# Performance work log

Measured on AMD Instinct MI355X. Metric: run time of the kernel, lower is better.

The kernel has to match this reference:

```python
import jax, jax.numpy as jnp
import numpy as np

N_NODES = 50000
N_EDGES = 800000
D_IN = 128
D_OUT = 128
N_GRAPHS = 512
N_CONVS = 5
EPS = 1e-5


def setup_inputs() -> dict:
    key = jax.random.key(0)
    ks = jax.random.split(key, 8)
    x = jax.random.normal(ks[0], (N_NODES, D_IN), dtype=jnp.float32)
    edge_index = jax.random.randint(ks[1], (2, N_EDGES), 0, N_NODES, dtype=jnp.int32)
    batch = jnp.sort(jax.random.randint(ks[2], (N_NODES,), 0, N_GRAPHS, dtype=jnp.int32))
    s = 1.0 / np.sqrt(D_IN)
    W_rel = jax.random.normal(ks[3], (N_CONVS, D_OUT, D_IN), dtype=jnp.float32) * s
    b_rel = jax.random.normal(ks[4], (N_CONVS, D_OUT), dtype=jnp.float32) * s
    W_root = jax.random.normal(ks[5], (N_CONVS, D_OUT, D_IN), dtype=jnp.float32) * s
    gamma = jnp.ones((D_OUT,), dtype=jnp.float32)
    beta = jnp.zeros((D_OUT,), dtype=jnp.float32)
    Wc = jax.random.normal(ks[6], (96, D_OUT), dtype=jnp.float32) * (1.0 / np.sqrt(D_OUT))
    bc = jax.random.normal(ks[7], (96,), dtype=jnp.float32) * (1.0 / np.sqrt(D_OUT))
    return {"x": x, "edge_index": edge_index, "batch": batch, "i": 0,
            "W_rel": W_rel, "b_rel": b_rel, "W_root": W_root,
            "gamma": gamma, "beta": beta, "Wc": Wc, "bc": bc}


def reference(x, edge_index, batch, i, W_rel, b_rel, W_root, gamma, beta, Wc, bc):
    # --- 5 GraphConv branches, summed. GraphConv: lin_rel(sum_{j->i} x_j) + lin_root(x).
    # Sum over the 5 convs commutes with the linears, so fold the weights first.
    src, dst = edge_index[0], edge_index[1]
    agg = jax.ops.segment_sum(x[src], dst, num_segments=N_NODES)  # [N, D_in]
    Wr = jnp.sum(W_rel, axis=0)   # [D_out, D_in]
    Wt = jnp.sum(W_root, axis=0)  # [D_out, D_in]
    br = jnp.sum(b_rel, axis=0)   # [D_out]
    h = agg @ Wr.T + x @ Wt.T + br  # [N, D_out]
    # --- NodeLevelBatchNorm (training: batch stats over all nodes, biased var)
    mean = jnp.mean(h, axis=0)
    var = jnp.mean((h - mean) ** 2, axis=0)
    h = gamma * (h - mean) * jax.lax.rsqrt(var + EPS) + beta
    # --- global max pool over graphs, relu, classifier (i=0 -> no-dropout branch)
    pooled = jax.ops.segment_max(h, batch, num_segments=N_GRAPHS)  # [G, D_out]
    pooled = jax.nn.relu(pooled)
    return pooled @ Wc.T + bc  # [G, 96]
```

## Files before the change

### kernel.cpp

```cpp
#include <hip/hip_runtime.h>

#define EPS 1e-5f

constexpr int NN = 50000, NE = 800000, DD = 128, NG = 512, NC = 5, NO = 96;
constexpr int MAXB = 8192;
constexpr int NBUCK = 196;

typedef __attribute__((ext_vector_type(8))) short bf16x8;
typedef __attribute__((ext_vector_type(4))) float f32x4;

constexpr size_t HB   = 0;
constexpr size_t XB   = (size_t)NN * DD / 2;
constexpr size_t WB   = XB + (size_t)NN * DD / 2;
constexpr size_t BRO  = WB + DD * 256 / 2;
constexpr size_t CSUM = BRO + DD;
constexpr size_t CSQ  = CSUM + 4 * DD;
constexpr size_t POOL = CSQ + 4 * DD;
constexpr size_t ZLEN = 8 * DD + (size_t)NG * DD;
constexpr size_t GCNT = POOL + (size_t)NG * DD;
constexpr size_t ROFF = GCNT + 256;
constexpr size_t BSTOR= ROFF + NN + 1;
constexpr size_t CSR16= BSTOR + (size_t)NBUCK*MAXB;

constexpr int XCAST_B = NN * DD / 4 / 256;
constexpr int FOLD_B  = DD * DD / 256;
constexpr int BUCK_B  = (NE + 4095) / 4096;

static __device__ __forceinline__ unsigned short f2b(float f) {
    unsigned int u = __float_as_uint(f);
    return (unsigned short)((u + 0x7FFFu + ((u >> 16) & 1u)) >> 16);
}
static __device__ __forceinline__ float b2f(unsigned short h) {
    return __uint_as_float(((unsigned int)h) << 16);
}
static __device__ __forceinline__ unsigned fkey(float f) {
    unsigned u = __float_as_uint(f);
    return (u >> 31) ? ~u : (u | 0x80000000u);
}
static __device__ __forceinline__ float unfkey(unsigned k) {
    unsigned u = (k & 0x80000000u) ? (k ^ 0x80000000u) : ~k;
    return __uint_as_float(u);
}

__global__ __launch_bounds__(256) void k_prep(const float* __restrict__ x,
                                              const float* __restrict__ Wrel,
                                              const float* __restrict__ brel,
                                              const float* __restrict__ Wroot,
                                              const int* __restrict__ ei,
                                              float* __restrict__ ws, int* __restrict__ wi) {
    __shared__ int lcnt[256];
    __shared__ int lbase[256];
    int b = blockIdx.x, t = threadIdx.x;
    if (b < XCAST_B) {
        int i = b * 256 + t;
        float4 v = ((const float4*)x)[i];
        ushort4 o = {f2b(v.x), f2b(v.y), f2b(v.z), f2b(v.w)};
        ((ushort4*)(ws + XB))[i] = o;
    } else if (b < XCAST_B + FOLD_B) {
        int idx = (b - XCAST_B) * 256 + t;
        int k = idx >> 7, o = idx & 127;
        float wr = 0.f, wt = 0.f;
        for (int c = 0; c < NC; ++c) {
            wr += Wrel [c*DD*DD + o*DD + k];
            wt += Wroot[c*DD*DD + o*DD + k];
        }
        unsigned short* wb = (unsigned short*)(ws + WB);
        wb[o*256 + k]       = f2b(wr);
        wb[o*256 + 128 + k] = f2b(wt);
        if (k == 0) {
            float bias = 0.f;
            for (int c = 0; c < NC; ++c) bias += brel[c*DD + o];
            ws[BRO + o] = bias;
        }
    } else {
        int bb = b - XCAST_B - FOLD_B;
        lcnt[t] = 0;
        __syncthreads();
        int val[16], krk[16];
        #pragma unroll
        for (int j = 0; j < 16; ++j) {
            int e = bb * 4096 + j * 256 + t;
            krk[j] = -1;
            if (e < NE) {
                int d = ei[NE + e], s = ei[e];
                int key = d >> 8;
                int r = atomicAdd(&lcnt[key], 1);
                val[j] = s | ((d & 255) << 16);
                krk[j] = (key << 16) | r;
            }
        }
        __syncthreads();
        if (t < NBUCK && lcnt[t] > 0)
            lbase[t] = atomicAdd(&wi[GCNT + t], lcnt[t]);
        __syncthreads();
        #pragma unroll
        for (int j = 0; j < 16; ++j) {
            if (krk[j] >= 0) {
                int key = krk[j] >> 16, r = krk[j] & 0xFFFF;
                int p = lbase[key] + r;
                if (p < MAXB) wi[BSTOR + (size_t)key * MAXB + p] = val[j];
            }
        }
    }
}

__global__ __launch_bounds__(256) void k_sort(int* __restrict__ wi) {
    __shared__ int eds[MAXB];
    __shared__ unsigned short srt[MAXB];
    __shared__ int cnt[256], cnt2[256], lscan[256], gall[256];
    int t = threadIdx.x, b = blockIdx.x;
    for (size_t i = (size_t)b * 256 + t; i < ZLEN; i += (size_t)NBUCK * 256)
        wi[CSUM + i] = 0;
    int g = wi[GCNT + t];
    gall[t] = g; lscan[t] = g; cnt[t] = 0;
    __syncthreads();
    for (int off = 1; off < 256; off <<= 1) {
        int u = (t >= off) ? gall[t - off] : 0;
        __syncthreads();
        gall[t] += u;
        __syncthreads();
    }
    int base = gall[b] - lscan[b];
    int C = lscan[b]; if (C > MAXB) C = MAXB;
    __syncthreads();
    for (int i = t; i < C; i += 256) {
        int v = wi[BSTOR + (size_t)b * MAXB + i];
        eds[i] = v;
        atomicAdd(&cnt[v >> 16], 1);
    }
    __syncthreads();
    int cv = cnt[t];
    for (int off = 1; off < 256; off <<= 1) {
        int u = (t >= off) ? cnt[t - off] : 0;
        __syncthreads();
        cnt[t] += u;
        __syncthreads();
    }
    lscan[t] = cnt[t] - cv;
    cnt2[t] = 0;
    __syncthreads();
    int n = b * 256 + t;
    if (n < NN) wi[ROFF + n] = base + lscan[t];
    if (b == 0 && t == 0) wi[ROFF + NN] = NE;
    for (int i = t; i < C; i += 256) {
        int v = eds[i], k = v >> 16;
        int p = lscan[k] + atomicAdd(&cnt2[k], 1);
        srt[p] = (unsigned short)(v & 0xFFFF);
    }
    __syncthreads();
    unsigned short* csr = (unsigned short*)(wi + CSR16);
    for (int i = t; i < C; i += 256)
        csr[base + i] = srt[i];
}

__global__ __launch_bounds__(256) void k_gather(const int* __restrict__ wi,
                                                float* __restrict__ ws) {
    const unsigned short* xb = (const unsigned short*)(ws + XB);
    const unsigned short* csr = (const unsigned short*)(wi + CSR16);
    unsigned short* hb = (unsigned short*)(ws + HB);
    int tid = threadIdx.x;
    int n   = blockIdx.x * 16 + (tid >> 4);
    int sub = tid & 15;
    int c8  = sub * 8;
    if (n >= NN) return;
    int e0 = wi[ROFF + n], e1 = wi[ROFF + n + 1];
    int cnt = e1 - e0;
    float acc0[8] = {}, acc1[8] = {};
    int base = 0;
    for (; base + 16 <= cnt; base += 16) {
        int myE = (int)csr[e0 + base + sub];
        #pragma unroll
        for (int h = 0; h < 2; ++h) {
            bf16x8 v[8];
            #pragma unroll
            for (int j = 0; j < 8; ++j) {
                int s = __shfl(myE, h * 8 + j, 16);
                v[j] = *(const bf16x8*)&xb[(size_t)s * DD + c8];
            }
            #pragma unroll
            for (int j = 0; j < 8; ++j)
                #pragma unroll
                for (int c = 0; c < 8; ++c)
                    ((j & 1) ? acc1 : acc0)[c] += b2f((unsigned short)v[j][c]);
        }
    }
    int rem = cnt - base;
    if (rem > 0) {
        int myE = (sub < rem) ? (int)csr[e0 + base + sub] : 0;
        int j = 0;
        for (; j + 8 <= rem; j += 8) {
            bf16x8 v[8];
            #pragma unroll
            for (int q = 0; q < 8; ++q) {
                int s = __shfl(myE, j + q, 16);
                v[q] = *(const bf16x8*)&xb[(size_t)s * DD + c8];
            }
            #pragma unroll
            for (int q = 0; q < 8; ++q)
                #pragma unroll
                for (int c = 0; c < 8; ++c)
                    ((q & 1) ? acc1 : acc0)[c] += b2f((unsigned short)v[q][c]);
        }
        if (j + 4 <= rem) {
            bf16x8 v[4];
            #pragma unroll
            for (int q = 0; q < 4; ++q) {
                int s = __shfl(myE, j + q, 16);
                v[q] = *(const bf16x8*)&xb[(size_t)s * DD + c8];
            }
            #pragma unroll
            for (int q = 0; q < 4; ++q)
                #pragma unroll
                for (int c = 0; c < 8; ++c)
                    ((q & 1) ? acc1 : acc0)[c] += b2f((unsigned short)v[q][c]);
            j += 4;
        }
        for (; j < rem; ++j) {
            int s = __shfl(myE, j, 16);
            bf16x8 v = *(const bf16x8*)&xb[(size_t)s * DD + c8];
            #pragma unroll
            for (int c = 0; c < 8; ++c) acc0[c] += b2f((unsigned short)v[c]);
        }
    }
    bf16x8 o;
    #pragma unroll
    for (int c = 0; c < 8; ++c) o[c] = (short)f2b(acc0[c] + acc1[c]);
    *(bf16x8*)&hb[(size_t)n * DD + c8] = o;
}

__global__ __launch_bounds__(256, 2) void k_gemm(const int* __restrict__ batch,
                                                 float* __restrict__ ws) {
    __shared__ __align__(16) unsigned short Bs[DD * 256];
    __shared__ float sSum[128], sSq[128];
    __shared__ int batchS[64];
    __shared__ unsigned maxS[8][128];
    const unsigned short* hb = (const unsigned short*)(ws + HB);
    const unsigned short* xb = (const unsigned short*)(ws + XB);
    unsigned* poolU = (unsigned*)(ws + POOL);
    int tid  = threadIdx.x;
    {
        const float4* wbg = (const float4*)(ws + WB);
        #pragma unroll
        for (int i = 0; i < 16; ++i) {
            int idx = i * 256 + tid;
            float4 v = wbg[idx];
            int byte = idx << 4;
            int col  = byte >> 9;
            int swb  = byte ^ ((col & 7) << 4);
            *(float4*)((char*)Bs + swb) = v;
        }
    }
    if (tid < 128) { sSum[tid] = 0.f; sSq[tid] = 0.f; }
    for (int i = tid; i < 8 * 128; i += 256) ((unsigned*)maxS)[i] = 0u;
    if (tid < 64) {
        int r = blockIdx.x * 64 + tid; if (r > NN - 1) r = NN - 1;
        batchS[tid] = batch[r];
    }
    __syncthreads();
    int gBase = batchS[0];
    int wave = tid >> 6, lane = tid & 63;
    int quad = lane >> 4, l16 = lane & 15;
    int cw = wave * 32;
    auto ldb = [&](int col, int kt) -> bf16x8 {
        int byte = (col << 9) + (kt << 6) + (quad << 4);
        byte ^= ((col & 7) << 4);
        return *(const bf16x8*)((const char*)Bs + byte);
    };
    float bias[2] = { ws[BRO + cw + l16], ws[BRO + cw + 16 + l16] };
    float csum[2] = {}, csq[2] = {};
    #pragma unroll
    for (int rt = 0; rt < 4; ++rt) {
        int lbase = rt * 16;
        int row0 = blockIdx.x * 64 + lbase;
        int arow = row0 + l16; if (arow > NN - 1) arow = NN - 1;
        const unsigned short* aggRow = hb + (size_t)arow * DD;
        const unsigned short* xRow   = xb + (size_t)arow * DD;
        bf16x8 af[8];
        #pragma unroll
        for (int kt = 0; kt < 8; ++kt)
            af[kt] = *(const bf16x8*)((kt < 4 ? aggRow + kt*32 : xRow + kt*32 - 128) + quad*8);
        f32x4 acc[2] = {};
        #pragma unroll
        for (int kt = 0; kt < 8; ++kt) {
            bf16x8 b0 = ldb(cw + l16, kt);
            bf16x8 b1 = ldb(cw + 16 + l16, kt);
            acc[0] = __builtin_amdgcn_mfma_f32_16x16x32_bf16(af[kt], b0, acc[0], 0, 0, 0);
            acc[1] = __builtin_amdgcn_mfma_f32_16x16x32_bf16(af[kt], b1, acc[1], 0, 0, 0);
        }
        #pragma unroll
        for (int nt = 0; nt < 2; ++nt) {
            int col = cw + nt*16 + l16;
            #pragma unroll
            for (int r = 0; r < 4; ++r) {
                int lrow = lbase + quad*4 + r;
                int row  = row0 + quad*4 + r;
                float m = (row < NN) ? 1.f : 0.f;
                float v = acc[nt][r] + bias[nt];
                csum[nt] += v * m;
                csq[nt]  += v * v * m;
                int g   = batchS[lrow];
                int rel = g - gBase;
                unsigned key = (row < NN) ? fkey(v) : 0u;
                if (rel < 8) atomicMax(&maxS[rel][col], key);
                else         atomicMax(&poolU[(size_t)g * DD + col], key);
            }
        }
    }
    __syncthreads();
    int span = batchS[63] - gBase + 1; if (span > 8) span = 8;
    for (int i = tid; i < span * 128; i += 256) {
        unsigned k = maxS[i >> 7][i & 127];
        if (k) atomicMax(&poolU[(size_t)(gBase + (i >> 7)) * DD + (i & 127)], k);
    }
    #pragma unroll
    for (int nt = 0; nt < 2; ++nt) {
        int col = cw + nt*16 + l16;
        float cs = csum[nt], cq = csq[nt];
        cs += __shfl_xor(cs, 16); cs += __shfl_xor(cs, 32);
        cq += __shfl_xor(cq, 16); cq += __shfl_xor(cq, 32);
        if (quad == 0) { atomicAdd(&sSum[col], cs); atomicAdd(&sSq[col], cq); }
    }
    __syncthreads();
    if (tid < 128) {
        int slot = (blockIdx.x & 3) * DD;
        atomicAdd(&ws[CSUM + slot + tid], sSum[tid]);
        atomicAdd(&ws[CSQ  + slot + tid], sSq[tid]);
    }
}

__global__ __launch_bounds__(128) void k_out(const float* __restrict__ gamma,
                                             const float* __restrict__ beta,
                                             const float* __restrict__ Wc,
                                             const float* __restrict__ bc,
                                             const float* __restrict__ ws,
                                             float* __restrict__ out) {
    __shared__ float pS[128];
    int g = blockIdx.x, t = threadIdx.x;
    float s = ws[CSUM + t] + ws[CSUM + DD + t] + ws[CSUM + 2*DD + t] + ws[CSUM + 3*DD + t];
    float q = ws[CSQ  + t] + ws[CSQ  + DD + t] + ws[CSQ  + 2*DD + t] + ws[CSQ  + 3*DD + t];
    float mean = s * (1.0f / NN);
    float var  = q * (1.0f / NN) - mean * mean;
    float sc   = gamma[t] * rsqrtf(var + EPS);
    float sh   = beta[t] - sc * mean;
    unsigned k = ((const unsigned*)(ws + POOL))[(size_t)g * DD + t];
    float p = 0.f;
    if (k) p = fmaxf(unfkey(k) * sc + sh, 0.f);
    pS[t] = p;
    __syncthreads();
    if (t < NO) {
        float acc = bc[t];
        #pragma unroll 8
        for (int kk = 0; kk < DD; ++kk) acc += pS[kk] * Wc[t*DD + kk];
        out[g*NO + t] = acc;
    }
}

extern "C" void kernel_launch(void* const* d_in, const int* in_sizes, int n_in,
                              void* d_out, int out_size, void* d_ws, size_t ws_size,
                              hipStream_t stream) {
    const float* x     = (const float*)d_in[0];
    const int*   ei    = (const int*)  d_in[1];
    const int*   batch = (const int*)  d_in[2];
    const float* Wrel  = (const float*)d_in[4];
    const float* brel  = (const float*)d_in[5];
    const float* Wroot = (const float*)d_in[6];
    const float* gamma = (const float*)d_in[7];
    const float* beta  = (const float*)d_in[8];
    const float* Wc    = (const float*)d_in[9];
    const float* bc    = (const float*)d_in[10];
    float* ws  = (float*)d_ws;
    int*   wi  = (int*)d_ws;
    float* out = (float*)d_out;

    hipMemsetAsync(wi + GCNT, 0, 256 * sizeof(int), stream);

    k_prep  <<<XCAST_B + FOLD_B + BUCK_B, 256, 0, stream>>>(x, Wrel, brel, Wroot, ei, ws, wi);
    k_sort  <<<NBUCK, 256, 0, stream>>>(wi);
    k_gather<<<(NN + 15)/16, 256, 0, stream>>>(wi, ws);
    k_gemm  <<<(NN + 63)/64, 256, 0, stream>>>(batch, ws);
    k_out   <<<NG, 128, 0, stream>>>(gamma, beta, Wc, bc, ws, out);
}
```

Before: 181.1 us.

## Replace global bucket atomics with per-block count matrix and fuse output into GEMM tail

Edge bucketing no longer uses global atomic counters plus a memset. Each prep block writes its per-bucket counts into a 2D matrix and stores its edges in fixed-capacity slots. The sort kernel sums and scans these counts and finds each edge's source slot with a binary search. The final classifier kernel is folded into the GEMM kernel: the last 32 blocks to finish wait on a done counter and then compute the normalized pooled outputs. This removes one launch and the memset, at the cost of spin-waiting and silently dropping edges if a block's bucket count exceeds the 64-slot capacity.

```diff
diff --git a/kernel.cpp b/kernel.cpp
--- a/kernel.cpp
+++ b/kernel.cpp
@@ -5,6 +5,10 @@
 constexpr int NN = 50000, NE = 800000, DD = 128, NG = 512, NC = 5, NO = 96;
 constexpr int MAXB = 8192;
 constexpr int NBUCK = 196;
+constexpr int NPB   = 196;
+constexpr int CAP   = 64;
+constexpr int GEMM_V= (NN + 63) / 64;
+constexpr int FIN   = 32;
 
 typedef __attribute__((ext_vector_type(8))) short bf16x8;
 typedef __attribute__((ext_vector_type(4))) float f32x4;
@@ -16,11 +20,12 @@
 constexpr size_t CSUM = BRO + DD;
 constexpr size_t CSQ  = CSUM + 4 * DD;
 constexpr size_t POOL = CSQ + 4 * DD;
-constexpr size_t ZLEN = 8 * DD + (size_t)NG * DD;
-constexpr size_t GCNT = POOL + (size_t)NG * DD;
-constexpr size_t ROFF = GCNT + 256;
+constexpr size_t DONE = POOL + (size_t)NG * DD;
+constexpr size_t ZLEN = 8 * DD + (size_t)NG * DD + 8;
+constexpr size_t ROFF = DONE + 8;
 constexpr size_t BSTOR= ROFF + NN + 1;
-constexpr size_t CSR16= BSTOR + (size_t)NBUCK*MAXB;
+constexpr size_t CNT2D= BSTOR + (size_t)NBUCK * NPB * CAP;
+constexpr size_t CSR16= CNT2D + (size_t)NPB * 256;
 
 constexpr int XCAST_B = NN * DD / 4 / 256;
 constexpr int FOLD_B  = DD * DD / 256;
@@ -49,7 +54,6 @@
                                               const int* __restrict__ ei,
                                               float* __restrict__ ws, int* __restrict__ wi) {
     __shared__ int lcnt[256];
-    __shared__ int lbase[256];
     int b = blockIdx.x, t = threadIdx.x;
     if (b < XCAST_B) {
         int i = b * 256 + t;
@@ -90,15 +94,16 @@
             }
         }
         __syncthreads();
-        if (t < NBUCK && lcnt[t] > 0)
-            lbase[t] = atomicAdd(&wi[GCNT + t], lcnt[t]);
-        __syncthreads();
+        if (t < NBUCK) {
+            int c = lcnt[t];
+            wi[CNT2D + (size_t)bb * 256 + t] = c < CAP ? c : CAP;
+        }
         #pragma unroll
         for (int j = 0; j < 16; ++j) {
             if (krk[j] >= 0) {
                 int key = krk[j] >> 16, r = krk[j] & 0xFFFF;
-                int p = lbase[key] + r;
-                if (p < MAXB) wi[BSTOR + (size_t)key * MAXB + p] = val[j];
+                if (r < CAP)
+                    wi[BSTOR + ((size_t)key * NPB + bb) * CAP + r] = val[j];
             }
         }
     }
@@ -111,8 +116,10 @@
     int t = threadIdx.x, b = blockIdx.x;
     for (size_t i = (size_t)b * 256 + t; i < ZLEN; i += (size_t)NBUCK * 256)
         wi[CSUM + i] = 0;
-    int g = wi[GCNT + t];
-    gall[t] = g; lscan[t] = g; cnt[t] = 0;
+    int tot = 0;
+    if (t < NBUCK)
+        for (int bb = 0; bb < NPB; ++bb) tot += wi[CNT2D + (size_t)bb * 256 + t];
+    gall[t] = tot; lscan[t] = tot;
     __syncthreads();
     for (int off = 1; off < 256; off <<= 1) {
         int u = (t >= off) ? gall[t - off] : 0;
@@ -123,8 +130,26 @@
     int base = gall[b] - lscan[b];
     int C = lscan[b]; if (C > MAXB) C = MAXB;
     __syncthreads();
+    int myc = (t < NPB) ? wi[CNT2D + (size_t)t * 256 + b] : 0;
+    gall[t] = myc; cnt[t] = myc;
+    __syncthreads();
+    for (int off = 1; off < 256; off <<= 1) {
+        int u = (t >= off) ? gall[t - off] : 0;
+        __syncthreads();
+        gall[t] += u;
+        __syncthreads();
+    }
+    lscan[t] = gall[t] - cnt[t];
+    cnt[t] = 0;
+    __syncthreads();
     for (int i = t; i < C; i += 256) {
-        int v = wi[BSTOR + (size_t)b * MAXB + i];
+        int lo = 0, hi = NPB - 1;
+        #pragma unroll
+        for (int s8 = 0; s8 < 8; ++s8) {
+            int mid = (lo + hi + 1) >> 1;
+            if (lscan[mid] <= i) lo = mid; else hi = mid - 1;
+        }
+        int v = wi[BSTOR + ((size_t)b * NPB + lo) * CAP + (i - lscan[lo])];
         eds[i] = v;
         atomicAdd(&cnt[v >> 16], 1);
     }
@@ -229,14 +254,21 @@
 }
 
 __global__ __launch_bounds__(256, 2) void k_gemm(const int* __restrict__ batch,
-                                                 float* __restrict__ ws) {
+                                                 const float* __restrict__ gamma,
+                                                 const float* __restrict__ beta,
+                                                 const float* __restrict__ Wc,
+                                                 const float* __restrict__ bc,
+                                                 float* __restrict__ ws,
+                                                 float* __restrict__ out) {
     __shared__ __align__(16) unsigned short Bs[DD * 256];
     __shared__ float sSum[128], sSq[128];
     __shared__ int batchS[64];
     __shared__ unsigned maxS[8][128];
+    __shared__ int oldS;
     const unsigned short* hb = (const unsigned short*)(ws + HB);
     const unsigned short* xb = (const unsigned short*)(ws + XB);
     unsigned* poolU = (unsigned*)(ws + POOL);
+    int* done = (int*)ws + DONE;
     int tid  = threadIdx.x;
     {
         const float4* wbg = (const float4*)(ws + WB);
@@ -326,32 +358,43 @@
         atomicAdd(&ws[CSUM + slot + tid], sSum[tid]);
         atomicAdd(&ws[CSQ  + slot + tid], sSq[tid]);
     }
-}
-
-__global__ __launch_bounds__(128) void k_out(const float* __restrict__ gamma,
-                                             const float* __restrict__ beta,
-                                             const float* __restrict__ Wc,
-                                             const float* __restrict__ bc,
-                                             const float* __restrict__ ws,
-                                             float* __restrict__ out) {
-    __shared__ float pS[128];
-    int g = blockIdx.x, t = threadIdx.x;
-    float s = ws[CSUM + t] + ws[CSUM + DD + t] + ws[CSUM + 2*DD + t] + ws[CSUM + 3*DD + t];
-    float q = ws[CSQ  + t] + ws[CSQ  + DD + t] + ws[CSQ  + 2*DD + t] + ws[CSQ  + 3*DD + t];
+    __syncthreads();
+    if (tid == 0) {
+        __threadfence();
+        oldS = atomicAdd(done, 1);
+    }
+    __syncthreads();
+    int old = oldS;
+    if (old < GEMM_V - FIN) return;
+    if (tid == 0) {
+        while (atomicAdd(done, 0) < GEMM_V)
+            __builtin_amdgcn_s_sleep(8);
+        __threadfence();
+    }
+    __syncthreads();
+    int fin = old - (GEMM_V - FIN);
+    float* pS = (float*)Bs;
+    int half = tid >> 7, tt = tid & 127;
+    float s = ws[CSUM + tt] + ws[CSUM + DD + tt] + ws[CSUM + 2*DD + tt] + ws[CSUM + 3*DD + tt];
+    float q = ws[CSQ  + tt] + ws[CSQ  + DD + tt] + ws[CSQ  + 2*DD + tt] + ws[CSQ  + 3*DD + tt];
     float mean = s * (1.0f / NN);
     float var  = q * (1.0f / NN) - mean * mean;
-    float sc   = gamma[t] * rsqrtf(var + EPS);
-    float sh   = beta[t] - sc * mean;
-    unsigned k = ((const unsigned*)(ws + POOL))[(size_t)g * DD + t];
-    float p = 0.f;
-    if (k) p = fmaxf(unfkey(k) * sc + sh, 0.f);
-    pS[t] = p;
-    __syncthreads();
-    if (t < NO) {
-        float acc = bc[t];
-        #pragma unroll 8
-        for (int kk = 0; kk < DD; ++kk) acc += pS[kk] * Wc[t*DD + kk];
-        out[g*NO + t] = acc;
+    float sc   = gamma[tt] * rsqrtf(var + EPS);
+    float sh   = beta[tt] - sc * mean;
+    for (int i = 0; i < 16 / 2; ++i) {
+        int g = fin * 16 + i * 2 + half;
+        unsigned k = poolU[(size_t)g * DD + tt];
+        float p = 0.f;
+        if (k) p = fmaxf(unfkey(k) * sc + sh, 0.f);
+        pS[half * 128 + tt] = p;
+        __syncthreads();
+        if (tt < NO) {
+            float acc = bc[tt];
+            #pragma unroll 8
+            for (int kk = 0; kk < DD; ++kk) acc += pS[half * 128 + kk] * Wc[tt*DD + kk];
+            out[g*NO + tt] = acc;
+        }
+        __syncthreads();
     }
 }
 
@@ -372,11 +415,8 @@
     int*   wi  = (int*)d_ws;
     float* out = (float*)d_out;
 
-    hipMemsetAsync(wi + GCNT, 0, 256 * sizeof(int), stream);
-
     k_prep  <<<XCAST_B + FOLD_B + BUCK_B, 256, 0, stream>>>(x, Wrel, brel, Wroot, ei, ws, wi);
     k_sort  <<<NBUCK, 256, 0, stream>>>(wi);
     k_gather<<<(NN + 15)/16, 256, 0, stream>>>(wi, ws);
-    k_gemm  <<<(NN + 63)/64, 256, 0, stream>>>(batch, ws);
-    k_out   <<<NG, 128, 0, stream>>>(gamma, beta, Wc, bc, ws, out);
-}
+    k_gemm  <<<GEMM_V, 256, 0, stream>>>(batch, gamma, beta, Wc, bc, ws, out);
+}
```

After: 243.8 us. 34.6% more time.
